# Performance work log

Hardware: AMD Instinct MI355X
Metric: run time of the kernel (lower is better)

The kernel has to match this reference:

```python
import jax, jax.numpy as jnp
import numpy as np

N_NODES = 50000
N_EDGES = 500000
N_REL = 8
D = 128        # input_dim
A_DIM = 64     # attention_dim
D_OUT = 128    # output_dim


def setup_inputs() -> dict:
    key = jax.random.key(0)
    ks = jax.random.split(key, 10)
    h = jax.random.normal(ks[0], (N_NODES, D), jnp.float32)
    # relation gate tables: [R, 2*D, D]; first D rows act on dst (subject), last D on src (object)
    relations = jax.random.normal(ks[1], (N_REL, 2 * D, D), jnp.float32) * 0.05
    rel_attention = jax.random.normal(ks[2], (N_REL, A_DIM), jnp.float32) * 0.05
    W_a = jax.random.normal(ks[3], (A_DIM, 2 * D), jnp.float32) * 0.05
    b_a = jnp.zeros((A_DIM,), jnp.float32)
    W_lin = jax.random.normal(ks[4], (D_OUT, 2 * D), jnp.float32) * 0.05
    b_lin = jnp.zeros((D_OUT,), jnp.float32)
    src = jax.random.randint(ks[5], (N_EDGES,), 0, N_NODES, dtype=jnp.int32)
    dst = jax.random.randint(ks[6], (N_EDGES,), 0, N_NODES, dtype=jnp.int32)
    etype = jax.random.randint(ks[7], (N_EDGES,), 0, N_REL, dtype=jnp.int32)
    return {"h": h, "relations": relations, "rel_attention": rel_attention,
            "W_a": W_a, "b_a": b_a, "W_lin": W_lin, "b_lin": b_lin,
            "src": src, "dst": dst, "etype": etype}


def reference(h, relations, rel_attention, W_a, b_a, W_lin, b_lin, src, dst, etype):
    d = h.shape[-1]
    # --- gates: relation-indexed gather_mm (concat gate type) ---
    # Project every node through every relation once (R is small), then gather per edge.
    proj_dst = jnp.einsum('nd,rde->rne', h, relations[:, :d, :])   # [R, N, D] subject/dst side
    proj_src = jnp.einsum('nd,rde->rne', h, relations[:, d:, :])   # [R, N, D] object/src side
    gate = jax.nn.sigmoid(proj_dst[etype, dst] + proj_src[etype, src])  # [E, D]

    src_h = h[src]   # [E, D]
    dst_h = h[dst]   # [E, D]

    # --- gatv2 attention (predicates are zeroed in the module -> rel_attention[0]) ---
    a = jax.nn.leaky_relu(jnp.concatenate([dst_h, src_h], axis=-1) @ W_a.T + b_a)  # [E, A]
    score = (rel_attention[0] * a).sum(-1)  # [E]

    # --- edge_softmax over destination-node segments ---
    smax = jax.ops.segment_max(score, dst, num_segments=N_NODES)
    ex = jnp.exp(score - smax[dst])
    denom = jax.ops.segment_sum(ex, dst, num_segments=N_NODES)
    attn = ex / denom[dst]  # [E]

    # --- message = u_mul_e(h, attn*gate), reduce = sum over dst ---
    msg = src_h * (attn[:, None] * gate)                 # [E, D]
    h_N = jax.ops.segment_sum(msg, dst, num_segments=N_NODES)  # [N, D]

    # --- graphsage aggregate: LeakyReLU(W [h ; h_N] + b) ---
    out = jax.nn.leaky_relu(jnp.concatenate([h, h_N], axis=-1) @ W_lin.T + b_lin)
    return out
```

## Files before the change

### kernel.cpp

```cpp
#include <hip/hip_runtime.h>
#include <cstdint>
#include <cstddef>

constexpr int NNODES = 50000;
constexpr int NEDGES = 500000;
constexpr int NRELS  = 8;
constexpr int DIM    = 128;
constexpr int ADIM   = 64;
constexpr int TWOD   = 256;
constexpr int EPB    = 64;
constexpr float SLOPE = 0.01f;

constexpr int XPITCH = TWOD + 8;
constexpr int SPAD = NEDGES + 1024;

typedef __attribute__((ext_vector_type(8))) short short8;
typedef __attribute__((ext_vector_type(4))) float floatx4;

__device__ __forceinline__ unsigned short f2bf(float f) {
    unsigned u = __float_as_uint(f);
    unsigned r = u + 0x7FFFu + ((u >> 16) & 1u);
    return (unsigned short)(r >> 16);
}
__device__ __forceinline__ float bf2f(unsigned short b) {
    return __uint_as_float(((unsigned)b) << 16);
}
__device__ __forceinline__ float sigmoid_fast(float x) {
    return __builtin_amdgcn_rcpf(1.0f + __expf(-x));
}

__global__ void k_init(int* __restrict__ histD, int* __restrict__ cnts) {
    int i = blockIdx.x * blockDim.x + threadIdx.x;
    int stride = gridDim.x * blockDim.x;
    for (int idx = i; idx < NNODES; idx += stride) histD[idx] = 0;
    if (i < 16) cnts[i] = 0;
}

__global__ __launch_bounds__(256) void k_prep(const float* __restrict__ rel,
                                              const float* __restrict__ W_lin,
                                              const float* __restrict__ W_a,
                                              unsigned short* __restrict__ relT,
                                              unsigned short* __restrict__ Wl,
                                              unsigned short* __restrict__ Wa16) {
    __shared__ float ls[64][65];
    int b = blockIdx.x, t = threadIdx.x;
    if (b < 64) {
        int r = b >> 3, tile = b & 7;
        int d0 = (tile >> 1) * 64, o0 = (tile & 1) * 64;
        const float* rp = rel + ((size_t)r * TWOD + d0) * DIM + o0;
#pragma unroll
        for (int u = 0; u < 16; u++) {
            int v = u * 256 + t;
            int j = v & 63, i = v >> 6;
            ls[i][j] = rp[(size_t)i * DIM + j];
        }
        __syncthreads();
        unsigned short* wp = relT + ((size_t)r * DIM + o0) * TWOD + d0;
#pragma unroll
        for (int u = 0; u < 16; u++) {
            int v = u * 256 + t;
            int ii = v & 63, jj = v >> 6;
            wp[(size_t)jj * TWOD + ii] = f2bf(ls[ii][jj]);
        }
    } else {
        int idx = (b - 64) * 256 + t;
        if (idx < DIM * TWOD) {
            Wl[idx] = f2bf(W_lin[idx]);
        } else {
            int j = idx - DIM * TWOD;
            if (j < ADIM * TWOD) Wa16[j] = f2bf(W_a[j]);
        }
    }
}

__global__ void k_h16(const float* __restrict__ h, unsigned short* __restrict__ h16) {
    int i = blockIdx.x * 256 + threadIdx.x;
    if (i < NNODES * DIM / 8) {
        const float4* hp = (const float4*)(h + (size_t)i * 8);
        float4 a = hp[0], b = hp[1];
        union { unsigned short us[8]; short8 s8; } pk;
        pk.us[0] = f2bf(a.x); pk.us[1] = f2bf(a.y); pk.us[2] = f2bf(a.z); pk.us[3] = f2bf(a.w);
        pk.us[4] = f2bf(b.x); pk.us[5] = f2bf(b.y); pk.us[6] = f2bf(b.z); pk.us[7] = f2bf(b.w);
        *(short8*)&h16[(size_t)i * 8] = pk.s8;
    }
}

__global__ void k_hist2(const int* __restrict__ ety, const int* __restrict__ dst,
                        int* __restrict__ cnt, int* __restrict__ histD) {
    __shared__ int hist[NRELS];
    int t = threadIdx.x;
    if (t < NRELS) hist[t] = 0;
    __syncthreads();
    int e = blockIdx.x * 256 + t;
    if (e < NEDGES) {
        atomicAdd(&hist[ety[e]], 1);
        atomicAdd(&histD[dst[e]], 1);
    }
    __syncthreads();
    if (t < NRELS && hist[t] > 0) atomicAdd(&cnt[t], hist[t]);
}

__global__ __launch_bounds__(1024) void k_scan(const int* __restrict__ histD,
                                               int* __restrict__ row_ptr,
                                               int* __restrict__ cursorD,
                                               const int* __restrict__ cnt,
                                               int* __restrict__ offs,
                                               uint2* __restrict__ sMeta) {
    __shared__ int ls[1024];
    __shared__ int s_offs[NRELS + 1];
    __shared__ int s_cnt[NRELS];
    const int t = threadIdx.x;
    const int CH = (NNODES + 1023) / 1024;
    const int base = t * CH;
    int s = 0;
    for (int j = 0; j < CH; j++) { int i = base + j; if (i < NNODES) s += histD[i]; }
    ls[t] = s;
    __syncthreads();
    for (int off = 1; off < 1024; off <<= 1) {
        int v = (t >= off) ? ls[t - off] : 0;
        __syncthreads();
        ls[t] += v;
        __syncthreads();
    }
    int run = (t == 0) ? 0 : ls[t - 1];
    for (int j = 0; j < CH; j++) {
        int i = base + j;
        if (i < NNODES) { row_ptr[i] = run; cursorD[i] = 0; run += histD[i]; }
    }
    if (t == 1023) row_ptr[NNODES] = ls[1023];
    if (t == 0) {
        int off = 0;
        for (int r = 0; r < NRELS; r++) {
            offs[r] = off; s_offs[r] = off; s_cnt[r] = cnt[r];
            off += ((cnt[r] + EPB - 1) / EPB) * EPB;
        }
        s_offs[NRELS] = off;
    }
    __syncthreads();
#pragma unroll
    for (int r = 0; r < NRELS; r++) {
        int s0 = s_offs[r] + s_cnt[r];
        int e0 = s_offs[r + 1 > NRELS ? NRELS : r + 1];
        for (int idx = s0 + t; idx < e0; idx += 1024) sMeta[idx] = make_uint2(0xFFFFFFFFu, 0u);
    }
    for (int idx = s_offs[NRELS] + t; idx < SPAD; idx += 1024)
        sMeta[idx] = make_uint2(0xFFFFFFFFu, 0u);
}

__global__ void k_escatter(const int* __restrict__ ety, const int* __restrict__ src,
                           const int* __restrict__ dst, const int* __restrict__ row_ptr,
                           const int* __restrict__ offs,
                           int* __restrict__ cursorD, int* __restrict__ cursorE,
                           uint2* __restrict__ sMeta) {
    __shared__ int hist[NRELS];
    __shared__ int basew[NRELS];
    int t = threadIdx.x;
    if (t < NRELS) hist[t] = 0;
    __syncthreads();
    int e = blockIdx.x * 256 + t;
    int r = -1, rank = 0, sn = 0, dn = 0;
    if (e < NEDGES) {
        r = ety[e]; sn = src[e]; dn = dst[e];
        rank = atomicAdd(&hist[r], 1);
    }
    __syncthreads();
    if (t < NRELS && hist[t] > 0) basew[t] = atomicAdd(&cursorE[t], hist[t]);
    __syncthreads();
    if (e < NEDGES) {
        int s = offs[r] + basew[r] + rank;
        int pos = row_ptr[dn] + atomicAdd(&cursorD[dn], 1);
        sMeta[s] = make_uint2((unsigned)sn | ((unsigned)dn << 16), (unsigned)pos);
    }
}

__global__ __launch_bounds__(256, 4) void k_gate_msg(
    const unsigned short* __restrict__ h16, const unsigned short* __restrict__ relT,
    const unsigned short* __restrict__ Wa16,
    const uint2* __restrict__ sMeta, const float* __restrict__ b_a,
    const float* __restrict__ ratt, const int* __restrict__ offs,
    unsigned short* __restrict__ msgbuf, float* __restrict__ scoreP) {
    __shared__ unsigned short Xs[EPB * XPITCH];
    __shared__ int srcn_s[EPB];
    __shared__ int dstn_s[EPB];
    __shared__ int pos_s[EPB];
    __shared__ int val_s[EPB];
    __shared__ float scoreW[EPB][4];

    const int t = threadIdx.x;
    const int base = blockIdx.x * EPB;

    if (t < EPB) {
        uint2 m2 = sMeta[base + t];
        int valid = (m2.x != 0xFFFFFFFFu);
        val_s[t] = valid;
        srcn_s[t] = valid ? (int)(m2.x & 0xFFFFu) : 0;
        dstn_s[t] = valid ? (int)(m2.x >> 16) : 0;
        pos_s[t] = valid ? (int)m2.y : 0;
    }
    __syncthreads();
    if (!val_s[0]) return;

    int r = 0;
#pragma unroll
    for (int i = 1; i < NRELS; i++) if (base >= offs[i]) r = i;

#pragma unroll
    for (int u = 0; u < 8; u++) {
        int v = u * 256 + t;
        int i = v >> 5;
        int c = v & 31;
        int node = (c < 16) ? dstn_s[i] : srcn_s[i];
        *(short8*)&Xs[i * XPITCH + c * 8] = *(const short8*)&h16[(size_t)node * DIM + (c & 15) * 8];
    }

    const int wave = t >> 6;
    const int lane = t & 63;
    const int q = lane >> 4;
    const int l16 = lane & 15;
    const int o16 = wave * 16 + l16;

    const unsigned short* bp0 = relT + ((size_t)r * DIM + (wave * 2 + 0) * 16 + l16) * TWOD + q * 8;
    const unsigned short* bp1 = relT + ((size_t)r * DIM + (wave * 2 + 1) * 16 + l16) * TWOD + q * 8;
    const unsigned short* wb  = Wa16 + (size_t)o16 * TWOD + q * 8;

    short8 B0p[4], B1p[4], BSp[4];
#pragma unroll
    for (int ks = 0; ks < 4; ks++) {
        B0p[ks] = *(const short8*)(bp0 + ks * 32);
        B1p[ks] = *(const short8*)(bp1 + ks * 32);
        BSp[ks] = *(const short8*)(wb + ks * 32);
    }

    __syncthreads();

    floatx4 acc[4][2];
    floatx4 accS[4];
#pragma unroll
    for (int m = 0; m < 4; m++) {
        acc[m][0] = (floatx4)(0.0f);
        acc[m][1] = (floatx4)(0.0f);
        accS[m] = (floatx4)(0.0f);
    }

#pragma unroll
    for (int ks = 0; ks < 8; ks++) {
        short8 B0 = (ks < 4) ? B0p[ks & 3] : *(const short8*)(bp0 + ks * 32);
        short8 B1 = (ks < 4) ? B1p[ks & 3] : *(const short8*)(bp1 + ks * 32);
        short8 BS = (ks < 4) ? BSp[ks & 3] : *(const short8*)(wb + ks * 32);
        short8 Af[4];
        const unsigned short* xb = &Xs[l16 * XPITCH + ks * 32 + q * 8];
#pragma unroll
        for (int m = 0; m < 4; m++) Af[m] = *(const short8*)(xb + m * 16 * XPITCH);
#pragma unroll
        for (int m = 0; m < 4; m++) {
            acc[m][0] = __builtin_amdgcn_mfma_f32_16x16x32_bf16(Af[m], B0, acc[m][0], 0, 0, 0);
            acc[m][1] = __builtin_amdgcn_mfma_f32_16x16x32_bf16(Af[m], B1, acc[m][1], 0, 0, 0);
            accS[m]   = __builtin_amdgcn_mfma_f32_16x16x32_bf16(Af[m], BS, accS[m], 0, 0, 0);
        }
    }

    __syncthreads();

    {
        float ba = b_a[o16];
        float ra = ratt[o16];
#pragma unroll
        for (int m = 0; m < 4; m++) {
#pragma unroll
            for (int rg = 0; rg < 4; rg++) {
                float v = accS[m][rg] + ba;
                v = v > 0.0f ? v : SLOPE * v;
                v *= ra;
#pragma unroll
                for (int off = 8; off > 0; off >>= 1) v += __shfl_xor(v, off, 16);
                if (l16 == 0) scoreW[m * 16 + q * 4 + rg][wave] = v;
            }
        }
    }

#pragma unroll
    for (int m = 0; m < 4; m++) {
        int ib = m * 16 + q * 4;
#pragma unroll
        for (int nn = 0; nn < 2; nn++) {
            int o = (wave * 2 + nn) * 16 + l16;
#pragma unroll
            for (int rg = 0; rg < 4; rg++) {
                int i = ib + rg;
                float g = sigmoid_fast(acc[m][nn][rg]);
                float sh = bf2f(Xs[i * XPITCH + DIM + o]);
                Xs[i * XPITCH + o] = f2bf(sh * g);
            }
        }
    }
    __syncthreads();

#pragma unroll
    for (int u = 0; u < 4; u++) {
        int v = u * 256 + t;
        int i = v >> 4;
        int c = v & 15;
        if (!val_s[i]) continue;
        short8 val = *(const short8*)&Xs[i * XPITCH + c * 8];
        *(short8*)&msgbuf[(size_t)pos_s[i] * DIM + c * 8] = val;
    }
    if (t < EPB && val_s[t]) {
        scoreP[pos_s[t]] = scoreW[t][0] + scoreW[t][1] + scoreW[t][2] + scoreW[t][3];
    }
}

__global__ __launch_bounds__(256) void k_aggr(const unsigned short* __restrict__ msgbuf,
                                              const float* __restrict__ scoreP,
                                              const int* __restrict__ row_ptr,
                                              unsigned short* __restrict__ hN16) {
    int n = blockIdx.x * 4 + (threadIdx.x >> 6);
    int lane = threadIdx.x & 63;
    if (n >= NNODES) return;
    int p0 = row_ptr[n], p1 = row_ptr[n + 1];
    float a0 = 0.0f, a1 = 0.0f;
    if (p0 < p1) {
        float mx = -3.0e38f;
        for (int p = p0 + lane; p < p1; p += 64) mx = fmaxf(mx, scoreP[p]);
#pragma unroll
        for (int off = 32; off > 0; off >>= 1) mx = fmaxf(mx, __shfl_xor(mx, off));
        float sum = 0.0f;
        for (int p = p0 + lane; p < p1; p += 64) sum += __expf(scoreP[p] - mx);
#pragma unroll
        for (int off = 32; off > 0; off >>= 1) sum += __shfl_xor(sum, off);
        int p = p0;
        const unsigned short* mb = msgbuf + (size_t)lane * 2;
        for (; p + 4 <= p1; p += 4) {
            float w0 = __expf(scoreP[p + 0] - mx);
            float w1 = __expf(scoreP[p + 1] - mx);
            float w2 = __expf(scoreP[p + 2] - mx);
            float w3 = __expf(scoreP[p + 3] - mx);
            unsigned v0 = *(const unsigned*)&mb[(size_t)(p + 0) * DIM];
            unsigned v1 = *(const unsigned*)&mb[(size_t)(p + 1) * DIM];
            unsigned v2 = *(const unsigned*)&mb[(size_t)(p + 2) * DIM];
            unsigned v3 = *(const unsigned*)&mb[(size_t)(p + 3) * DIM];
            a0 = fmaf(w0, bf2f((unsigned short)(v0 & 0xFFFFu)), a0);
            a1 = fmaf(w0, bf2f((unsigned short)(v0 >> 16)), a1);
            a0 = fmaf(w1, bf2f((unsigned short)(v1 & 0xFFFFu)), a0);
            a1 = fmaf(w1, bf2f((unsigned short)(v1 >> 16)), a1);
            a0 = fmaf(w2, bf2f((unsigned short)(v2 & 0xFFFFu)), a0);
            a1 = fmaf(w2, bf2f((unsigned short)(v2 >> 16)), a1);
            a0 = fmaf(w3, bf2f((unsigned short)(v3 & 0xFFFFu)), a0);
            a1 = fmaf(w3, bf2f((unsigned short)(v3 >> 16)), a1);
        }
        for (; p < p1; p++) {
            float w = __expf(scoreP[p] - mx);
            unsigned v = *(const unsigned*)&mb[(size_t)p * DIM];
            a0 = fmaf(w, bf2f((unsigned short)(v & 0xFFFFu)), a0);
            a1 = fmaf(w, bf2f((unsigned short)(v >> 16)), a1);
        }
        float inv = __builtin_amdgcn_rcpf(sum);
        a0 *= inv; a1 *= inv;
    }
    unsigned o = (unsigned)f2bf(a0) | ((unsigned)f2bf(a1) << 16);
    *(unsigned*)&hN16[(size_t)n * DIM + lane * 2] = o;
}

__global__ __launch_bounds__(256) void k_out(const unsigned short* __restrict__ h16,
                                             const unsigned short* __restrict__ hN16,
                                             const unsigned short* __restrict__ Wl,
                                             const float* __restrict__ b_lin,
                                             float* __restrict__ out) {
    __shared__ unsigned short Xs[EPB * XPITCH];
    const int t = threadIdx.x;
    const int nb = blockIdx.x * 64;

#pragma unroll
    for (int u = 0; u < 8; u++) {
        int v = u * 256 + t;
        int i = v >> 5;
        int c = v & 31;
        int n = nb + i;
        if (n >= NNODES) n = NNODES - 1;
        const unsigned short* srcp = (c < 16) ? h16 : hN16;
        *(short8*)&Xs[i * XPITCH + c * 8] = *(const short8*)&srcp[(size_t)n * DIM + (c & 15) * 8];
    }

    const int wave = t >> 6;
    const int lane = t & 63;
    const int q = lane >> 4;
    const int l16 = lane & 15;

    short8 Bf[2][8];
#pragma unroll
    for (int nn = 0; nn < 2; nn++) {
        int o = (wave * 2 + nn) * 16 + l16;
        const unsigned short* bp = Wl + (size_t)o * TWOD + q * 8;
#pragma unroll
        for (int ks = 0; ks < 8; ks++) Bf[nn][ks] = *(const short8*)(bp + ks * 32);
    }

    __syncthreads();

    floatx4 acc[4][2];
#pragma unroll
    for (int m = 0; m < 4; m++)
#pragma unroll
        for (int nn = 0; nn < 2; nn++) acc[m][nn] = (floatx4)(0.0f);

#pragma unroll
    for (int ks = 0; ks < 8; ks++) {
        short8 Af[4];
        const unsigned short* xb = &Xs[l16 * XPITCH + ks * 32 + q * 8];
#pragma unroll
        for (int m = 0; m < 4; m++) Af[m] = *(const short8*)(xb + m * 16 * XPITCH);
#pragma unroll
        for (int m = 0; m < 4; m++)
#pragma unroll
            for (int nn = 0; nn < 2; nn++)
                acc[m][nn] = __builtin_amdgcn_mfma_f32_16x16x32_bf16(Af[m], Bf[nn][ks], acc[m][nn], 0, 0, 0);
    }

#pragma unroll
    for (int m = 0; m < 4; m++) {
        int ib = m * 16 + q * 4;
#pragma unroll
        for (int nn = 0; nn < 2; nn++) {
            int o = (wave * 2 + nn) * 16 + l16;
            float bl = b_lin[o];
#pragma unroll
            for (int rg = 0; rg < 4; rg++) {
                int n = nb + ib + rg;
                if (n < NNODES) {
                    float val = acc[m][nn][rg] + bl;
                    val = val > 0.0f ? val : SLOPE * val;
                    out[(size_t)n * DIM + o] = val;
                }
            }
        }
    }
}

extern "C" void kernel_launch(void* const* d_in, const int* in_sizes, int n_in,
                              void* d_out, int out_size, void* d_ws, size_t ws_size,
                              hipStream_t stream) {
    const float* h     = (const float*)d_in[0];
    const float* rel   = (const float*)d_in[1];
    const float* ratt  = (const float*)d_in[2];
    const float* W_a   = (const float*)d_in[3];
    const float* b_a   = (const float*)d_in[4];
    const float* W_lin = (const float*)d_in[5];
    const float* b_lin = (const float*)d_in[6];
    const int* src = (const int*)d_in[7];
    const int* dst = (const int*)d_in[8];
    const int* ety = (const int*)d_in[9];
    float* out = (float*)d_out;

    float* scoreP = (float*)d_ws;
    unsigned short* h16  = (unsigned short*)(scoreP + NEDGES);
    unsigned short* hN16 = h16 + (size_t)NNODES * DIM;
    unsigned short* relT = hN16 + (size_t)NNODES * DIM;
    unsigned short* Wl   = relT + (size_t)NRELS * DIM * TWOD;
    unsigned short* Wa16 = Wl + (size_t)DIM * TWOD;
    uint2* sMeta = (uint2*)(Wa16 + (size_t)ADIM * TWOD);
    int* row_ptr = (int*)(sMeta + SPAD);
    int* histD   = row_ptr + (NNODES + 1);
    int* cursorD = histD + NNODES;
    int* cnts    = cursorD + NNODES;
    int* offs    = cnts + 16;
    unsigned short* msgbuf = (unsigned short*)(((uintptr_t)(offs + 8) + 255) & ~(uintptr_t)255);

    k_init<<<196, 256, 0, stream>>>(histD, cnts);
    k_prep<<<64 + (DIM * TWOD + ADIM * TWOD + 255) / 256, 256, 0, stream>>>(
        rel, W_lin, W_a, relT, Wl, Wa16);
    k_h16<<<(NNODES * DIM / 8 + 255) / 256, 256, 0, stream>>>(h, h16);
    k_hist2<<<(NEDGES + 255) / 256, 256, 0, stream>>>(ety, dst, cnts, histD);
    k_scan<<<1, 1024, 0, stream>>>(histD, row_ptr, cursorD, cnts, offs, sMeta);
    k_escatter<<<(NEDGES + 255) / 256, 256, 0, stream>>>(
        ety, src, dst, row_ptr, offs, cursorD, cnts + 8, sMeta);
    k_gate_msg<<<(NEDGES + 8 * EPB + EPB - 1) / EPB, 256, 0, stream>>>(
        h16, relT, Wa16, sMeta, b_a, ratt, offs, msgbuf, scoreP);
    k_aggr<<<(NNODES + 3) / 4, 256, 0, stream>>>(msgbuf, scoreP, row_ptr, hN16);
    k_out<<<(NNODES + 63) / 64, 256, 0, stream>>>(h16, hN16, Wl, b_lin, out);
}
```

Measured before the change: 481.5 us.

## Sort edges by (relation, destination) via per-bucket histogram and two-level scan

Replaces the per-relation block-local bucketing of edges with a full counting sort keyed on (relation, dst node): a histogram over R*N buckets, a two-level parallel exclusive scan, and a scatter using per-bucket cursors. Within each relation segment, edges are now grouped by destination, which should improve locality of the gather and write patterns in the gate/message kernel. It adds an extra scan kernel, clears 800K counters, and performs more global atomics, which costs extra preprocessing time.

```diff
diff --git a/kernel.cpp b/kernel.cpp
--- a/kernel.cpp
+++ b/kernel.cpp
@@ -13,6 +13,8 @@
 
 constexpr int XPITCH = TWOD + 8;
 constexpr int SPAD = NEDGES + 1024;
+constexpr int SCAN_CHUNK = 1000;
+constexpr int NB_SCAN = NRELS * NNODES / SCAN_CHUNK;
 
 typedef __attribute__((ext_vector_type(8))) short short8;
 typedef __attribute__((ext_vector_type(4))) float floatx4;
@@ -29,11 +31,15 @@
     return __builtin_amdgcn_rcpf(1.0f + __expf(-x));
 }
 
-__global__ void k_init(int* __restrict__ histD, int* __restrict__ cnts) {
+__global__ void k_init(int* __restrict__ histD, int* __restrict__ histRD,
+                       int* __restrict__ cursorRD) {
     int i = blockIdx.x * blockDim.x + threadIdx.x;
     int stride = gridDim.x * blockDim.x;
     for (int idx = i; idx < NNODES; idx += stride) histD[idx] = 0;
-    if (i < 16) cnts[i] = 0;
+    for (int idx = i; idx < NRELS * NNODES; idx += stride) {
+        histRD[idx] = 0;
+        cursorRD[idx] = 0;
+    }
 }
 
 __global__ __launch_bounds__(256) void k_prep(const float* __restrict__ rel,
@@ -86,30 +92,86 @@
 }
 
 __global__ void k_hist2(const int* __restrict__ ety, const int* __restrict__ dst,
-                        int* __restrict__ cnt, int* __restrict__ histD) {
-    __shared__ int hist[NRELS];
-    int t = threadIdx.x;
-    if (t < NRELS) hist[t] = 0;
-    __syncthreads();
-    int e = blockIdx.x * 256 + t;
+                        int* __restrict__ histRD, int* __restrict__ histD) {
+    int e = blockIdx.x * 256 + threadIdx.x;
     if (e < NEDGES) {
-        atomicAdd(&hist[ety[e]], 1);
-        atomicAdd(&histD[dst[e]], 1);
-    }
-    __syncthreads();
-    if (t < NRELS && hist[t] > 0) atomicAdd(&cnt[t], hist[t]);
-}
-
-__global__ __launch_bounds__(1024) void k_scan(const int* __restrict__ histD,
-                                               int* __restrict__ row_ptr,
-                                               int* __restrict__ cursorD,
-                                               const int* __restrict__ cnt,
-                                               int* __restrict__ offs,
-                                               uint2* __restrict__ sMeta) {
+        int r = ety[e], dn = dst[e];
+        atomicAdd(&histRD[r * NNODES + dn], 1);
+        atomicAdd(&histD[dn], 1);
+    }
+}
+
+__global__ __launch_bounds__(256) void k_scanA(int* __restrict__ histRD,
+                                               int* __restrict__ blockSums) {
+    __shared__ int part[256];
+    int b = blockIdx.x, t = threadIdx.x;
+    int base = b * SCAN_CHUNK;
+    int i0 = t * 4;
+    int v[4]; int s = 0;
+#pragma unroll
+    for (int j = 0; j < 4; j++) {
+        int i = i0 + j;
+        v[j] = (i < SCAN_CHUNK) ? histRD[base + i] : 0;
+        s += v[j];
+    }
+    part[t] = s;
+    __syncthreads();
+    for (int off = 1; off < 256; off <<= 1) {
+        int x = (t >= off) ? part[t - off] : 0;
+        __syncthreads();
+        part[t] += x;
+        __syncthreads();
+    }
+    int run = (t == 0) ? 0 : part[t - 1];
+#pragma unroll
+    for (int j = 0; j < 4; j++) {
+        int i = i0 + j;
+        if (i < SCAN_CHUNK) { histRD[base + i] = run; run += v[j]; }
+    }
+    if (t == 255) blockSums[b] = part[255];
+}
+
+__global__ __launch_bounds__(1024) void k_scanB(const int* __restrict__ blockSums,
+                                                int* __restrict__ bp2,
+                                                const int* __restrict__ histD,
+                                                int* __restrict__ row_ptr,
+                                                int* __restrict__ cursorD,
+                                                int* __restrict__ offs,
+                                                uint2* __restrict__ sMeta) {
     __shared__ int ls[1024];
     __shared__ int s_offs[NRELS + 1];
     __shared__ int s_cnt[NRELS];
+    __shared__ int s_adj[NRELS];
     const int t = threadIdx.x;
+
+    ls[t] = (t < NB_SCAN) ? blockSums[t] : 0;
+    __syncthreads();
+    for (int off = 1; off < 1024; off <<= 1) {
+        int v = (t >= off) ? ls[t - off] : 0;
+        __syncthreads();
+        ls[t] += v;
+        __syncthreads();
+    }
+    if (t == 0) {
+        const int BPB = NNODES / SCAN_CHUNK;
+        int off = 0;
+        for (int r = 0; r < NRELS; r++) {
+            int sf0 = (r == 0) ? 0 : ls[BPB * r - 1];
+            int sf1 = ls[BPB * (r + 1) - 1];
+            int cnt = sf1 - sf0;
+            offs[r] = off; s_offs[r] = off; s_cnt[r] = cnt;
+            s_adj[r] = off - sf0;
+            off += ((cnt + EPB - 1) / EPB) * EPB;
+        }
+        s_offs[NRELS] = off;
+    }
+    __syncthreads();
+    if (t < NB_SCAN) {
+        int sf = (t == 0) ? 0 : ls[t - 1];
+        bp2[t] = sf + s_adj[t / (NNODES / SCAN_CHUNK)];
+    }
+    __syncthreads();
+
     const int CH = (NNODES + 1023) / 1024;
     const int base = t * CH;
     int s = 0;
@@ -128,19 +190,12 @@
         if (i < NNODES) { row_ptr[i] = run; cursorD[i] = 0; run += histD[i]; }
     }
     if (t == 1023) row_ptr[NNODES] = ls[1023];
-    if (t == 0) {
-        int off = 0;
-        for (int r = 0; r < NRELS; r++) {
-            offs[r] = off; s_offs[r] = off; s_cnt[r] = cnt[r];
-            off += ((cnt[r] + EPB - 1) / EPB) * EPB;
-        }
-        s_offs[NRELS] = off;
-    }
-    __syncthreads();
+    __syncthreads();
+
 #pragma unroll
     for (int r = 0; r < NRELS; r++) {
         int s0 = s_offs[r] + s_cnt[r];
-        int e0 = s_offs[r + 1 > NRELS ? NRELS : r + 1];
+        int e0 = s_offs[r + 1];
         for (int idx = s0 + t; idx < e0; idx += 1024) sMeta[idx] = make_uint2(0xFFFFFFFFu, 0u);
     }
     for (int idx = s_offs[NRELS] + t; idx < SPAD; idx += 1024)
@@ -149,28 +204,17 @@
 
 __global__ void k_escatter(const int* __restrict__ ety, const int* __restrict__ src,
                            const int* __restrict__ dst, const int* __restrict__ row_ptr,
-                           const int* __restrict__ offs,
-                           int* __restrict__ cursorD, int* __restrict__ cursorE,
+                           const int* __restrict__ histRD, const int* __restrict__ bp2,
+                           int* __restrict__ cursorRD, int* __restrict__ cursorD,
                            uint2* __restrict__ sMeta) {
-    __shared__ int hist[NRELS];
-    __shared__ int basew[NRELS];
-    int t = threadIdx.x;
-    if (t < NRELS) hist[t] = 0;
-    __syncthreads();
-    int e = blockIdx.x * 256 + t;
-    int r = -1, rank = 0, sn = 0, dn = 0;
-    if (e < NEDGES) {
-        r = ety[e]; sn = src[e]; dn = dst[e];
-        rank = atomicAdd(&hist[r], 1);
-    }
-    __syncthreads();
-    if (t < NRELS && hist[t] > 0) basew[t] = atomicAdd(&cursorE[t], hist[t]);
-    __syncthreads();
-    if (e < NEDGES) {
-        int s = offs[r] + basew[r] + rank;
-        int pos = row_ptr[dn] + atomicAdd(&cursorD[dn], 1);
-        sMeta[s] = make_uint2((unsigned)sn | ((unsigned)dn << 16), (unsigned)pos);
-    }
+    int e = blockIdx.x * 256 + threadIdx.x;
+    if (e >= NEDGES) return;
+    int r = ety[e], sn = src[e], dn = dst[e];
+    int idx = r * NNODES + dn;
+    int rank = atomicAdd(&cursorRD[idx], 1);
+    int slot = histRD[idx] + bp2[idx / SCAN_CHUNK] + rank;
+    int pos = row_ptr[dn] + atomicAdd(&cursorD[dn], 1);
+    sMeta[slot] = make_uint2((unsigned)sn | ((unsigned)dn << 16), (unsigned)pos);
 }
 
 __global__ __launch_bounds__(256, 4) void k_gate_msg(
@@ -463,15 +507,20 @@
     int* cnts    = cursorD + NNODES;
     int* offs    = cnts + 16;
     unsigned short* msgbuf = (unsigned short*)(((uintptr_t)(offs + 8) + 255) & ~(uintptr_t)255);
-
-    k_init<<<196, 256, 0, stream>>>(histD, cnts);
+    int* histRD    = (int*)msgbuf;
+    int* cursorRD  = histRD + NRELS * NNODES;
+    int* blockSums = cursorRD + NRELS * NNODES;
+    int* bp2       = blockSums + 512;
+
+    k_init<<<1024, 256, 0, stream>>>(histD, histRD, cursorRD);
     k_prep<<<64 + (DIM * TWOD + ADIM * TWOD + 255) / 256, 256, 0, stream>>>(
         rel, W_lin, W_a, relT, Wl, Wa16);
     k_h16<<<(NNODES * DIM / 8 + 255) / 256, 256, 0, stream>>>(h, h16);
-    k_hist2<<<(NEDGES + 255) / 256, 256, 0, stream>>>(ety, dst, cnts, histD);
-    k_scan<<<1, 1024, 0, stream>>>(histD, row_ptr, cursorD, cnts, offs, sMeta);
+    k_hist2<<<(NEDGES + 255) / 256, 256, 0, stream>>>(ety, dst, histRD, histD);
+    k_scanA<<<NB_SCAN, 256, 0, stream>>>(histRD, blockSums);
+    k_scanB<<<1, 1024, 0, stream>>>(blockSums, bp2, histD, row_ptr, cursorD, offs, sMeta);
     k_escatter<<<(NEDGES + 255) / 256, 256, 0, stream>>>(
-        ety, src, dst, row_ptr, offs, cursorD, cnts + 8, sMeta);
+        ety, src, dst, row_ptr, histRD, bp2, cursorRD, cursorD, sMeta);
     k_gate_msg<<<(NEDGES + 8 * EPB + EPB - 1) / EPB, 256, 0, stream>>>(
         h16, relT, Wa16, sMeta, b_a, ratt, offs, msgbuf, scoreP);
     k_aggr<<<(NNODES + 3) / 4, 256, 0, stream>>>(msgbuf, scoreP, row_ptr, hN16);
```

Result: no change. 490.2 us (median of 2 runs) (+1.8%).
